# Kernel optimization log

Hardware: AMD Instinct MI355X
Metric: run time of the kernel (lower is better)

The kernel has to match this reference:

```python
import jax, jax.numpy as jnp
import numpy as np

N_ORDER = 64
SEQ_LEN = 4096
BATCH = 256


def _hippo_scale_buffers(N: int, L: int):
    """Build bilinear-discretized scaled-Legendre (HiPPO-LegS) transition buffers."""
    q = np.arange(N, dtype=np.float64)
    col, row = np.meshgrid(q, q)  # col[i,j]=j, row[i,j]=i
    r = 2 * q + 1
    M = -(np.where(row >= col, r, 0) - np.diag(q))
    T = np.sqrt(np.diag(2 * q + 1))
    A = T @ M @ np.linalg.inv(T)              # (N,N) continuous-time A
    Bv = np.sqrt(2 * q + 1)                   # diag(T) -> continuous-time B vector
    t = np.arange(1, L + 1, dtype=np.float64)
    A_sc = A[None, :, :] / t[:, None, None]   # (L,N,N)
    B_sc = Bv[None, :] / t[:, None]           # (L,N)
    I = np.eye(N, dtype=np.float64)
    Mm = I[None] - 0.5 * A_sc
    Nn = I[None] + 0.5 * A_sc
    A_d = np.linalg.solve(Mm, Nn)                        # (L,N,N)
    B_d = np.linalg.solve(Mm, B_sc[..., None])[..., 0]   # (L,N)
    return A_d.astype(np.float32), B_d.astype(np.float32)


def setup_inputs() -> dict:
    key = jax.random.key(0)
    inputs = jax.random.normal(key, (SEQ_LEN, BATCH), dtype=jnp.float32)
    A_np, B_np = _hippo_scale_buffers(N_ORDER, SEQ_LEN)
    return {
        "inputs": inputs,
        "A_stacked": jnp.asarray(A_np),   # (L,N,N)
        "B_stacked": jnp.asarray(B_np),   # (L,N)
    }


def reference(inputs, A_stacked, B_stacked):
    """x_t = A_t @ x_{t-1} + B_t * inputs_t, x_{-1} = 0. Returns (L, B, N)."""
    L = inputs.shape[0]
    # u[t, b, :] = inputs[t, b] * B_stacked[t, :]
    u = inputs[..., None] * B_stacked[:L, None, :]  # (L,B,N)

    def step(x, au):
        A_t, u_t = au                                  # (N,N), (B,N)
        x = u_t + jnp.einsum('ij,bj->bi', A_t, x)      # (B,N)
        return x, x

    x0 = jnp.zeros(u.shape[1:], dtype=u.dtype)
    _, xs = jax.lax.scan(step, x0, (A_stacked[:L], u))
    return xs  # (L,B,N)
```

## Files before the change

### kernel.cpp

```cpp
#include <hip/hip_runtime.h>
#include <cstdint>


#define TID ((int)threadIdx.x)

typedef _Float16 half8 __attribute__((ext_vector_type(8)));
typedef _Float16 half4v __attribute__((ext_vector_type(4)));
typedef float f32x4 __attribute__((ext_vector_type(4)));

constexpr int SUBL  = 16;
constexpr int PAD   = 68;

constexpr size_t WS_W = 0;
constexpr size_t WS_Q = 262144;
constexpr size_t WS_P = WS_Q + 1048576;
constexpr size_t WS_Z = WS_P + 262144;
constexpr size_t WS_H = WS_Z + 1048576;
constexpr size_t OLD_WS_FLOATS = WS_H + 1048576;

constexpr int SLOT   = 20480;
constexpr int APITCH = 144;
constexpr int AL_OFF = 9216;
constexpr int BV_OFF = 18432;
constexpr int U_OFF  = 18688;
constexpr size_t AWS_BYTES = (size_t)4096 * SLOT;

__device__ __forceinline__ void stage64x64(const float* __restrict__ g, float* __restrict__ l) {
#pragma unroll
  for (int r = 0; r < 4; ++r) {
    int id = TID + 256 * r;
    int i = id >> 4, j0 = (id & 15) << 2;
    *reinterpret_cast<float4*>(&l[i * PAD + j0]) =
        *reinterpret_cast<const float4*>(&g[i * 64 + j0]);
  }
}

__device__ __forceinline__ void matmul_tile(const float* __restrict__ Ml,
                                            const float* __restrict__ Al,
                                            float* __restrict__ Dl,
                                            int i_lo, int i_hi) {
  float acc[4][4];
#pragma unroll
  for (int a = 0; a < 4; ++a)
#pragma unroll
    for (int b = 0; b < 4; ++b) acc[a][b] = 0.f;
  const int j0 = i_hi << 2;
#pragma unroll
  for (int kq = 0; kq < 16; ++kq) {
    const int k0 = kq << 2;
    float4 mf[4], af[4];
#pragma unroll
    for (int a = 0; a < 4; ++a)
      mf[a] = *reinterpret_cast<const float4*>(&Ml[(i_lo + 16 * a) * PAD + k0]);
#pragma unroll
    for (int kk = 0; kk < 4; ++kk)
      af[kk] = *reinterpret_cast<const float4*>(&Al[(k0 + kk) * PAD + j0]);
#pragma unroll
    for (int a = 0; a < 4; ++a) {
      acc[a][0] += mf[a].x * af[0].x + mf[a].y * af[1].x + mf[a].z * af[2].x + mf[a].w * af[3].x;
      acc[a][1] += mf[a].x * af[0].y + mf[a].y * af[1].y + mf[a].z * af[2].y + mf[a].w * af[3].y;
      acc[a][2] += mf[a].x * af[0].z + mf[a].y * af[1].z + mf[a].z * af[2].z + mf[a].w * af[3].z;
      acc[a][3] += mf[a].x * af[0].w + mf[a].y * af[1].w + mf[a].z * af[2].w + mf[a].w * af[3].w;
    }
  }
#pragma unroll
  for (int a = 0; a < 4; ++a)
    *reinterpret_cast<float4*>(&Dl[(i_lo + 16 * a) * PAD + j0]) =
        make_float4(acc[a][0], acc[a][1], acc[a][2], acc[a][3]);
}

__global__ __launch_bounds__(256) void k1_fused(const float* __restrict__ Ag,
                                                const float* __restrict__ Bg,
                                                const float* __restrict__ inp,
                                                unsigned char* __restrict__ Aws,
                                                float* __restrict__ W,
                                                float* __restrict__ Qw) {
  __shared__ float Ms[2][64 * PAD];
  __shared__ float As[2][64 * PAD];
  __shared__ float Bvs[2][64];
  const int c = blockIdx.x;
  const int i_lo = TID & 15, i_hi = TID >> 4;
  const int r_i0 = TID >> 4;
  const int r_j0 = (TID & 15) << 2;

  for (int idx = TID; idx < 64 * PAD; idx += 256) Ms[0][idx] = 0.f;

  float4 pc[4];
  float4 bvc = make_float4(0.f, 0.f, 0.f, 0.f);
  {
    const float* g = Ag + (size_t)(c * SUBL + SUBL - 1) * 4096;
#pragma unroll
    for (int r = 0; r < 4; ++r)
      pc[r] = *reinterpret_cast<const float4*>(&g[(r_i0 + 16 * r) * 64 + r_j0]);
    if (TID < 16)
      bvc = *reinterpret_cast<const float4*>(&Bg[(size_t)(c * SUBL + SUBL - 1) * 64 + TID * 4]);
  }
  __syncthreads();
  if (TID < 64) Ms[0][TID * PAD + TID] = 1.f;
#pragma unroll
  for (int r = 0; r < 4; ++r)
    *reinterpret_cast<float4*>(&As[0][(r_i0 + 16 * r) * PAD + r_j0]) = pc[r];
  if (TID < 16) *reinterpret_cast<float4*>(&Bvs[0][TID * 4]) = bvc;
  __syncthreads();

  int cur = 0, ab = 0;
  for (int k = SUBL - 1; k >= 0; --k) {
    const int t = c * SUBL + k;
    unsigned char* slot = Aws + (size_t)t * SLOT;
    float4 pn[4];
    float4 bvn = make_float4(0.f, 0.f, 0.f, 0.f);
    if (k > 0) {
      const float* g = Ag + (size_t)(t - 1) * 4096;
#pragma unroll
      for (int r = 0; r < 4; ++r)
        pn[r] = *reinterpret_cast<const float4*>(&g[(r_i0 + 16 * r) * 64 + r_j0]);
      if (TID < 16)
        bvn = *reinterpret_cast<const float4*>(&Bg[(size_t)(t - 1) * 64 + TID * 4]);
    }
    if (TID >= 64 && TID < 128) {
      int q = TID - 64;
      *reinterpret_cast<float4*>(slot + U_OFF + q * 16) =
          *reinterpret_cast<const float4*>(inp + (size_t)t * 256 + q * 4);
    }
    if (TID < 16) *reinterpret_cast<float4*>(slot + BV_OFF + TID * 16) = bvc;
    if (TID < 64) {
      float wv = 0.f;
#pragma unroll
      for (int kq = 0; kq < 16; ++kq) {
        float4 m = *reinterpret_cast<const float4*>(&Ms[cur][TID * PAD + kq * 4]);
        float4 b = *reinterpret_cast<const float4*>(&Bvs[ab][kq * 4]);
        wv += m.x * b.x + m.y * b.y + m.z * b.z + m.w * b.w;
      }
      W[t * 64 + TID] = wv;
    }
#pragma unroll
    for (int r = 0; r < 4; ++r) {
      float vv[4] = {pc[r].x, pc[r].y, pc[r].z, pc[r].w};
      half4v hh, ll;
#pragma unroll
      for (int e = 0; e < 4; ++e) {
        _Float16 h = (_Float16)vv[e];
        hh[e] = h;
        ll[e] = (_Float16)(vv[e] - (float)h);
      }
      const int row = r_i0 + 16 * r;
      *reinterpret_cast<half4v*>(slot + row * APITCH + r_j0 * 2) = hh;
      *reinterpret_cast<half4v*>(slot + AL_OFF + row * APITCH + r_j0 * 2) = ll;
    }
    if (TID < 64) {
      half8 z = {};
      *reinterpret_cast<half8*>(slot + TID * APITCH + 128) = z;
      *reinterpret_cast<half8*>(slot + AL_OFF + TID * APITCH + 128) = z;
    }
    matmul_tile(Ms[cur], As[ab], Ms[cur ^ 1], i_lo, i_hi);
    if (k > 0) {
#pragma unroll
      for (int r = 0; r < 4; ++r)
        *reinterpret_cast<float4*>(&As[ab ^ 1][(r_i0 + 16 * r) * PAD + r_j0]) = pn[r];
      if (TID < 16) *reinterpret_cast<float4*>(&Bvs[ab ^ 1][TID * 4]) = bvn;
#pragma unroll
      for (int r = 0; r < 4; ++r) pc[r] = pn[r];
      bvc = bvn;
    }
    __syncthreads();
    cur ^= 1;
    ab ^= 1;
  }
#pragma unroll
  for (int r = 0; r < 4; ++r) {
    int id = TID + 256 * r;
    int i = id >> 4, j0 = (id & 15) << 2;
    *reinterpret_cast<float4*>(&Qw[(size_t)c * 4096 + i * 64 + j0]) =
        *reinterpret_cast<const float4*>(&Ms[cur][i * PAD + j0]);
  }
}

__global__ __launch_bounds__(256) void k1_suffix(const float* __restrict__ Ag,
                                                 const float* __restrict__ Bg,
                                                 float* __restrict__ W,
                                                 float* __restrict__ Qw) {
  __shared__ float Ms[2][64 * PAD];
  __shared__ float As[64 * PAD];
  __shared__ float Bvs[64];
  const int c = blockIdx.x;
  const int i_lo = TID & 15, i_hi = TID >> 4;
  for (int idx = TID; idx < 64 * PAD; idx += 256) Ms[0][idx] = 0.f;
  __syncthreads();
  if (TID < 64) Ms[0][TID * PAD + TID] = 1.f;
  int cur = 0;
  for (int k = SUBL - 1; k >= 0; --k) {
    const int t = c * SUBL + k;
    stage64x64(Ag + (size_t)t * 4096, As);
    if (TID < 16)
      *reinterpret_cast<float4*>(&Bvs[TID * 4]) =
          *reinterpret_cast<const float4*>(&Bg[t * 64 + TID * 4]);
    __syncthreads();
    if (TID < 64) {
      float wv = 0.f;
#pragma unroll
      for (int kq = 0; kq < 16; ++kq) {
        float4 m = *reinterpret_cast<const float4*>(&Ms[cur][TID * PAD + kq * 4]);
        float4 b = *reinterpret_cast<const float4*>(&Bvs[kq * 4]);
        wv += m.x * b.x + m.y * b.y + m.z * b.z + m.w * b.w;
      }
      W[t * 64 + TID] = wv;
    }
    matmul_tile(Ms[cur], As, Ms[cur ^ 1], i_lo, i_hi);
    __syncthreads();
    cur ^= 1;
  }
#pragma unroll
  for (int r = 0; r < 4; ++r) {
    int id = TID + 256 * r;
    int i = id >> 4, j0 = (id & 15) << 2;
    *reinterpret_cast<float4*>(&Qw[(size_t)c * 4096 + i * 64 + j0]) =
        *reinterpret_cast<const float4*>(&Ms[cur][i * PAD + j0]);
  }
}

__global__ __launch_bounds__(256) void k1b_combine(const float* __restrict__ Qw,
                                                   float* __restrict__ W,
                                                   float* __restrict__ Pw) {
  __shared__ float R[2][64 * PAD];
  __shared__ float Qs[64 * PAD];
  __shared__ float wm[16 * PAD];
  const int s = blockIdx.x;
  const int i_lo = TID & 15, i_hi = TID >> 4;
  int cur = 0;
  for (int m = 3; m >= 0; --m) {
    const int c = 4 * s + m;
    stage64x64(Qw + (size_t)c * 4096, Qs);
    {
      int tt = TID >> 4, i0 = (TID & 15) << 2;
      *reinterpret_cast<float4*>(&wm[tt * PAD + i0]) =
          *reinterpret_cast<const float4*>(&W[(size_t)(c * 16 + tt) * 64 + i0]);
    }
    __syncthreads();
    if (m < 3) {
      float acc[4] = {0.f, 0.f, 0.f, 0.f};
#pragma unroll
      for (int kq = 0; kq < 16; ++kq) {
        const int k0 = kq << 2;
        float4 wf = *reinterpret_cast<const float4*>(&wm[i_hi * PAD + k0]);
#pragma unroll
        for (int a = 0; a < 4; ++a) {
          float4 rf = *reinterpret_cast<const float4*>(&R[cur][(i_lo + 16 * a) * PAD + k0]);
          acc[a] += rf.x * wf.x + rf.y * wf.y + rf.z * wf.z + rf.w * wf.w;
        }
      }
#pragma unroll
      for (int a = 0; a < 4; ++a)
        W[(size_t)(c * 16 + i_hi) * 64 + i_lo + 16 * a] = acc[a];
      matmul_tile(R[cur], Qs, R[cur ^ 1], i_lo, i_hi);
    } else {
#pragma unroll
      for (int r = 0; r < 4; ++r) {
        int id = TID + 256 * r;
        int i = id >> 4, j0 = (id & 15) << 2;
        *reinterpret_cast<float4*>(&R[cur ^ 1][i * PAD + j0]) =
            *reinterpret_cast<const float4*>(&Qs[i * PAD + j0]);
      }
    }
    __syncthreads();
    cur ^= 1;
  }
#pragma unroll
  for (int r = 0; r < 4; ++r) {
    int id = TID + 256 * r;
    int i = id >> 4, j0 = (id & 15) << 2;
    *reinterpret_cast<float4*>(&Pw[(size_t)s * 4096 + i * 64 + j0]) =
        *reinterpret_cast<const float4*>(&R[cur][i * PAD + j0]);
  }
}

__global__ __launch_bounds__(256) void k1c_zgemm(const float* __restrict__ inp,
                                                 const float* __restrict__ W,
                                                 float* __restrict__ Zw) {
  __shared__ float inT[64 * PAD];
  __shared__ float wm[64 * PAD];
  const int s = blockIdx.x >> 2, g = blockIdx.x & 3;
  const int b0 = 64 * g, t0 = s * 64;
  const int i_lo = TID & 15, i_hi = TID >> 4;
#pragma unroll
  for (int r = 0; r < 4; ++r) {
    int id = TID + 256 * r;
    int tl = id >> 4, b4 = (id & 15) << 2;
    float4 v = *reinterpret_cast<const float4*>(&inp[(size_t)(t0 + tl) * 256 + b0 + b4]);
    inT[(b4 + 0) * PAD + tl] = v.x;
    inT[(b4 + 1) * PAD + tl] = v.y;
    inT[(b4 + 2) * PAD + tl] = v.z;
    inT[(b4 + 3) * PAD + tl] = v.w;
  }
#pragma unroll
  for (int r = 0; r < 4; ++r) {
    int id = TID + 256 * r;
    int tl = id >> 4, i0 = (id & 15) << 2;
    *reinterpret_cast<float4*>(&wm[tl * PAD + i0]) =
        *reinterpret_cast<const float4*>(&W[(size_t)(t0 + tl) * 64 + i0]);
  }
  __syncthreads();
  float acc[4][4];
#pragma unroll
  for (int a = 0; a < 4; ++a)
#pragma unroll
    for (int q = 0; q < 4; ++q) acc[a][q] = 0.f;
  const int j0c = i_hi << 2;
#pragma unroll
  for (int kq = 0; kq < 16; ++kq) {
    const int k0 = kq << 2;
    float4 bf[4], wf[4];
#pragma unroll
    for (int a = 0; a < 4; ++a)
      bf[a] = *reinterpret_cast<const float4*>(&inT[(i_lo + 16 * a) * PAD + k0]);
#pragma unroll
    for (int kk = 0; kk < 4; ++kk)
      wf[kk] = *reinterpret_cast<const float4*>(&wm[(k0 + kk) * PAD + j0c]);
#pragma unroll
    for (int a = 0; a < 4; ++a) {
      acc[a][0] += bf[a].x * wf[0].x + bf[a].y * wf[1].x + bf[a].z * wf[2].x + bf[a].w * wf[3].x;
      acc[a][1] += bf[a].x * wf[0].y + bf[a].y * wf[1].y + bf[a].z * wf[2].y + bf[a].w * wf[3].y;
      acc[a][2] += bf[a].x * wf[0].z + bf[a].y * wf[1].z + bf[a].z * wf[2].z + bf[a].w * wf[3].z;
      acc[a][3] += bf[a].x * wf[0].w + bf[a].y * wf[1].w + bf[a].z * wf[2].w + bf[a].w * wf[3].w;
    }
  }
  __syncthreads();
#pragma unroll
  for (int a = 0; a < 4; ++a)
    *reinterpret_cast<float4*>(&wm[(i_lo + 16 * a) * PAD + j0c]) =
        make_float4(acc[a][0], acc[a][1], acc[a][2], acc[a][3]);
  __syncthreads();
#pragma unroll
  for (int r = 0; r < 4; ++r) {
    int id = TID + 256 * r;
    int bl = id >> 4, i0 = (id & 15) << 2;
    *reinterpret_cast<float4*>(&Zw[(size_t)s * 16384 + (b0 + bl) * 64 + i0]) =
        *reinterpret_cast<const float4*>(&wm[bl * PAD + i0]);
  }
}

__global__ __launch_bounds__(256) void k2_carry(const float* __restrict__ Pw,
                                                const float* __restrict__ Zw,
                                                float* __restrict__ Hw) {
  __shared__ float Pt[64 * PAD];
  __shared__ float xb[4 * PAD];
  const int g = blockIdx.x;
  const int bl = TID >> 6, i = TID & 63;
  const int bg = 4 * g + bl;
  const int ir = TID >> 4, j0 = (TID & 15) << 2;
  for (int idx = TID; idx < 4 * PAD; idx += 256) xb[idx] = 0.f;
  float4 p0[4];
#pragma unroll
  for (int r = 0; r < 4; ++r)
    p0[r] = *reinterpret_cast<const float4*>(&Pw[(ir + 16 * r) * 64 + j0]);
  float zc = Zw[(size_t)bg * 64 + i];
#pragma unroll
  for (int r = 0; r < 4; ++r) {
    int row = ir + 16 * r;
    Pt[(j0 + 0) * PAD + row] = p0[r].x;
    Pt[(j0 + 1) * PAD + row] = p0[r].y;
    Pt[(j0 + 2) * PAD + row] = p0[r].z;
    Pt[(j0 + 3) * PAD + row] = p0[r].w;
  }
  __syncthreads();
  float h = 0.f;
  for (int s = 0; s < 64; ++s) {
    float4 pn[4];
    float zn = 0.f;
    if (s < 63) {
#pragma unroll
      for (int r = 0; r < 4; ++r)
        pn[r] = *reinterpret_cast<const float4*>(
            &Pw[(size_t)(s + 1) * 4096 + (ir + 16 * r) * 64 + j0]);
      zn = Zw[(size_t)(s + 1) * 16384 + bg * 64 + i];
    }
    Hw[(size_t)s * 16384 + bg * 64 + i] = h;
    float acc = zc;
#pragma unroll
    for (int jq = 0; jq < 16; ++jq) {
      const int jj = jq << 2;
      float4 xf = *reinterpret_cast<const float4*>(&xb[bl * PAD + jj]);
      acc += Pt[(jj + 0) * PAD + i] * xf.x + Pt[(jj + 1) * PAD + i] * xf.y +
             Pt[(jj + 2) * PAD + i] * xf.z + Pt[(jj + 3) * PAD + i] * xf.w;
    }
    h = acc;
    __syncthreads();
    xb[bl * PAD + i] = h;
    if (s < 63) {
#pragma unroll
      for (int r = 0; r < 4; ++r) {
        int row = ir + 16 * r;
        Pt[(j0 + 0) * PAD + row] = pn[r].x;
        Pt[(j0 + 1) * PAD + row] = pn[r].y;
        Pt[(j0 + 2) * PAD + row] = pn[r].z;
        Pt[(j0 + 3) * PAD + row] = pn[r].w;
      }
      zc = zn;
    }
    __syncthreads();
  }
}

__global__ __launch_bounds__(256) void k3_final(const float* __restrict__ Ag,
                                                const float* __restrict__ Bg,
                                                const float* __restrict__ inp,
                                                const float* __restrict__ Hw,
                                                float* __restrict__ out) {
  __shared__ float As[64 * PAD];
  __shared__ float xs[64 * PAD];
  __shared__ float Bvs[64];
  __shared__ float ins[64];
  const int s = blockIdx.x >> 2, g = blockIdx.x & 3;
  const int b0 = 64 * g;
  const int i_lo = TID & 15, i_hi = TID >> 4;
#pragma unroll
  for (int r = 0; r < 4; ++r) {
    int id = TID + 256 * r;
    int bl = id >> 4, i0 = (id & 15) << 2;
    *reinterpret_cast<float4*>(&xs[bl * PAD + i0]) =
        *reinterpret_cast<const float4*>(&Hw[(size_t)s * 16384 + (b0 + bl) * 64 + i0]);
  }
  for (int k = 0; k < 64; ++k) {
    const int t = s * 64 + k;
    stage64x64(Ag + (size_t)t * 4096, As);
    if (TID < 16)
      *reinterpret_cast<float4*>(&Bvs[TID * 4]) =
          *reinterpret_cast<const float4*>(&Bg[t * 64 + TID * 4]);
    if (TID >= 64 && TID < 80) {
      int q = TID - 64;
      *reinterpret_cast<float4*>(&ins[q * 4]) =
          *reinterpret_cast<const float4*>(&inp[(size_t)t * 256 + b0 + q * 4]);
    }
    __syncthreads();
    float acc[4][4];
#pragma unroll
    for (int a = 0; a < 4; ++a)
#pragma unroll
      for (int r = 0; r < 4; ++r) acc[a][r] = 0.f;
#pragma unroll
    for (int jq = 0; jq < 16; ++jq) {
      const int j0 = jq << 2;
      float4 af[4], xf[4];
#pragma unroll
      for (int a = 0; a < 4; ++a)
        af[a] = *reinterpret_cast<const float4*>(&As[(i_lo + 16 * a) * PAD + j0]);
#pragma unroll
      for (int r = 0; r < 4; ++r)
        xf[r] = *reinterpret_cast<const float4*>(&xs[(i_hi + 16 * r) * PAD + j0]);
#pragma unroll
      for (int a = 0; a < 4; ++a)
#pragma unroll
        for (int r = 0; r < 4; ++r)
          acc[a][r] += af[a].x * xf[r].x + af[a].y * xf[r].y + af[a].z * xf[r].z + af[a].w * xf[r].w;
    }
    float bv[4], ui[4];
#pragma unroll
    for (int a = 0; a < 4; ++a) bv[a] = Bvs[i_lo + 16 * a];
#pragma unroll
    for (int r = 0; r < 4; ++r) ui[r] = ins[i_hi + 16 * r];
#pragma unroll
    for (int a = 0; a < 4; ++a)
#pragma unroll
      for (int r = 0; r < 4; ++r) acc[a][r] += bv[a] * ui[r];
    __syncthreads();
#pragma unroll
    for (int r = 0; r < 4; ++r)
#pragma unroll
      for (int a = 0; a < 4; ++a)
        xs[(i_hi + 16 * r) * PAD + i_lo + 16 * a] = acc[a][r];
    __syncthreads();
#pragma unroll
    for (int r = 0; r < 4; ++r) {
      int id = TID + 256 * r;
      int bl = id >> 4, i0 = (id & 15) << 2;
      *reinterpret_cast<float4*>(&out[((size_t)t * 256 + b0 + bl) * 64 + i0]) =
          *reinterpret_cast<const float4*>(&xs[bl * PAD + i0]);
    }
  }
}

__device__ __forceinline__ void gload_lds16(const void* g, void* l) {
  __builtin_amdgcn_global_load_lds(
      (const __attribute__((address_space(1))) unsigned int*)g,
      (__attribute__((address_space(3))) unsigned int*)l, 16, 0, 0);
}

constexpr int XROWS  = 32;
constexpr int LDS_XH = 2 * SLOT;
constexpr int LDS_XL = LDS_XH + XROWS * APITCH;
constexpr int LDS_SZ = LDS_XL + XROWS * APITCH;

__global__ __launch_bounds__(256, 2) void k3_mfma(const unsigned char* __restrict__ Aws,
                                                  const float* __restrict__ Hw,
                                                  float* __restrict__ out) {
  __shared__ __align__(16) unsigned char sm[LDS_SZ];
  const int blk = blockIdx.x;
  const int s = (blk & 7) | ((blk >> 6) << 3);
  const int g = (blk >> 3) & 7;
  const int b0 = g << 5;
  const int lane = TID & 63, wave = TID >> 6;
  const int lm = lane & 15, quad = lane >> 4;
  const int wm = wave >> 1, wn = wave & 1;

#pragma unroll
  for (int r = 0; r < 2; ++r) {
    int id = TID + (r << 8);
    int bl = id >> 4, j0 = (id & 15) << 2;
    float4 v = *reinterpret_cast<const float4*>(
        &Hw[(size_t)s * 16384 + (size_t)(b0 + bl) * 64 + j0]);
    float vv[4] = {v.x, v.y, v.z, v.w};
    half4v hh, ll;
#pragma unroll
    for (int e = 0; e < 4; ++e) {
      _Float16 h = (_Float16)vv[e];
      hh[e] = h;
      ll[e] = (_Float16)(vv[e] - (float)h);
    }
    *reinterpret_cast<half4v*>(sm + LDS_XH + bl * APITCH + (j0 << 1)) = hh;
    *reinterpret_cast<half4v*>(sm + LDS_XL + bl * APITCH + (j0 << 1)) = ll;
  }

  const size_t t0 = (size_t)s * 64;
  {
    const unsigned char* gsl = Aws + t0 * SLOT;
#pragma unroll
    for (int r = 0; r < 5; ++r) {
      int off = ((r << 2) + wave) << 10;
      gload_lds16(gsl + off + lane * 16, sm + off);
    }
  }

  int aoff[2][2], xoffh[2], xoffl[2], woff[2];
#pragma unroll
  for (int mt = 0; mt < 2; ++mt)
#pragma unroll
    for (int kt = 0; kt < 2; ++kt)
      aoff[mt][kt] = ((wm << 5) + (mt << 4) + lm) * APITCH + (((kt << 5) + (quad << 3)) << 1);
#pragma unroll
  for (int kt = 0; kt < 2; ++kt) {
    int o = ((wn << 4) + lm) * APITCH + (((kt << 5) + (quad << 3)) << 1);
    xoffh[kt] = LDS_XH + o;
    xoffl[kt] = LDS_XL + o;
  }
#pragma unroll
  for (int mt = 0; mt < 2; ++mt)
    woff[mt] = ((wn << 4) + lm) * APITCH + (((wm << 5) + (mt << 4) + (quad << 2)) << 1);

  __syncthreads();

  int cur = 0;
  for (int k = 0; k < 64; ++k) {
    const unsigned char* ab = sm + cur * SLOT;
    if (k < 63) {
      const unsigned char* gsl = Aws + (t0 + k + 1) * SLOT;
      unsigned char* lb = sm + (cur ^ 1) * SLOT;
#pragma unroll
      for (int r = 0; r < 5; ++r) {
        int off = ((r << 2) + wave) << 10;
        gload_lds16(gsl + off + lane * 16, lb + off);
      }
    }
    half8 fa[2][2], fal[2][2], fxh[2], fxl[2];
#pragma unroll
    for (int mt = 0; mt < 2; ++mt)
#pragma unroll
      for (int kt = 0; kt < 2; ++kt) {
        fa[mt][kt]  = *reinterpret_cast<const half8*>(ab + aoff[mt][kt]);
        fal[mt][kt] = *reinterpret_cast<const half8*>(ab + AL_OFF + aoff[mt][kt]);
      }
#pragma unroll
    for (int kt = 0; kt < 2; ++kt) {
      fxh[kt] = *reinterpret_cast<const half8*>(sm + xoffh[kt]);
      fxl[kt] = *reinterpret_cast<const half8*>(sm + xoffl[kt]);
    }
    float4 bv[2];
#pragma unroll
    for (int mt = 0; mt < 2; ++mt)
      bv[mt] = *reinterpret_cast<const float4*>(
          ab + BV_OFF + (((wm << 5) + (mt << 4) + (quad << 2)) << 2));
    float uu = *reinterpret_cast<const float*>(
        ab + U_OFF + ((b0 + (wn << 4) + lm) << 2));

    f32x4 acc[2] = {};
#pragma unroll
    for (int mt = 0; mt < 2; ++mt)
#pragma unroll
      for (int kt = 0; kt < 2; ++kt) {
        acc[mt] = __builtin_amdgcn_mfma_f32_16x16x32_f16(fa[mt][kt],  fxh[kt], acc[mt], 0, 0, 0);
        acc[mt] = __builtin_amdgcn_mfma_f32_16x16x32_f16(fal[mt][kt], fxh[kt], acc[mt], 0, 0, 0);
        acc[mt] = __builtin_amdgcn_mfma_f32_16x16x32_f16(fa[mt][kt],  fxl[kt], acc[mt], 0, 0, 0);
      }
#pragma unroll
    for (int mt = 0; mt < 2; ++mt) {
      const float* bp = reinterpret_cast<const float*>(&bv[mt]);
#pragma unroll
      for (int e = 0; e < 4; ++e) acc[mt][e] += bp[e] * uu;
    }
    __syncthreads();
#pragma unroll
    for (int mt = 0; mt < 2; ++mt) {
      half4v hh, ll;
#pragma unroll
      for (int e = 0; e < 4; ++e) {
        float x = acc[mt][e];
        _Float16 h = (_Float16)x;
        hh[e] = h;
        ll[e] = (_Float16)(x - (float)h);
      }
      *reinterpret_cast<half4v*>(sm + LDS_XH + woff[mt]) = hh;
      *reinterpret_cast<half4v*>(sm + LDS_XL + woff[mt]) = ll;
      const int bglob = b0 + (wn << 4) + lm;
      const int irow = (wm << 5) + (mt << 4) + (quad << 2);
      *reinterpret_cast<float4*>(&out[(((t0 + k) << 8) + bglob) * 64 + irow]) =
          make_float4(acc[mt][0], acc[mt][1], acc[mt][2], acc[mt][3]);
    }
    __syncthreads();
    cur ^= 1;
  }
}

extern "C" void kernel_launch(void* const* d_in, const int* in_sizes, int n_in,
                              void* d_out, int out_size, void* d_ws, size_t ws_size,
                              hipStream_t stream) {
  const float* inputs = (const float*)d_in[0];
  const float* Ag     = (const float*)d_in[1];
  const float* Bg     = (const float*)d_in[2];
  float* out = (float*)d_out;

  const bool use_mfma = ws_size >= AWS_BYTES + OLD_WS_FLOATS * 4;
  unsigned char* Aws = (unsigned char*)d_ws;
  float* ws = (float*)((char*)d_ws + (use_mfma ? AWS_BYTES : 0));
  float* W  = ws + WS_W;
  float* Qw = ws + WS_Q;
  float* Pw = ws + WS_P;
  float* Zw = ws + WS_Z;
  float* Hw = ws + WS_H;

  if (use_mfma)
    k1_fused<<<256, 256, 0, stream>>>(Ag, Bg, inputs, Aws, W, Qw);
  else
    k1_suffix<<<256, 256, 0, stream>>>(Ag, Bg, W, Qw);
  k1b_combine<<<64, 256, 0, stream>>>(Qw, W, Pw);
  k1c_zgemm<<<256, 256, 0, stream>>>(inputs, W, Zw);
  k2_carry<<<64, 256, 0, stream>>>(Pw, Zw, Hw);
  if (use_mfma)
    k3_mfma<<<512, 256, 0, stream>>>(Aws, Hw, out);
  else
    k3_final<<<256, 256, 0, stream>>>(Ag, Bg, inputs, Hw, out);
}
```

Measured before the change: 581.7 us.

## Triple-buffer A slices and double-buffer state to halve barriers per step

Result: no change. 585.1 us (+0.6%).

```diff
diff --git a/kernel.cpp b/kernel.cpp
--- a/kernel.cpp
+++ b/kernel.cpp
@@ -341,13 +341,13 @@
 __global__ __launch_bounds__(256) void k2_carry(const float* __restrict__ Pw,
                                                 const float* __restrict__ Zw,
                                                 float* __restrict__ Hw) {
-  __shared__ float Pt[64 * PAD];
-  __shared__ float xb[4 * PAD];
+  __shared__ float Pt[2][64 * PAD];
+  __shared__ float xb[2][4 * PAD];
   const int g = blockIdx.x;
   const int bl = TID >> 6, i = TID & 63;
   const int bg = 4 * g + bl;
   const int ir = TID >> 4, j0 = (TID & 15) << 2;
-  for (int idx = TID; idx < 4 * PAD; idx += 256) xb[idx] = 0.f;
+  for (int idx = TID; idx < 4 * PAD; idx += 256) xb[0][idx] = 0.f;
   float4 p0[4];
 #pragma unroll
   for (int r = 0; r < 4; ++r)
@@ -356,14 +356,15 @@
 #pragma unroll
   for (int r = 0; r < 4; ++r) {
     int row = ir + 16 * r;
-    Pt[(j0 + 0) * PAD + row] = p0[r].x;
-    Pt[(j0 + 1) * PAD + row] = p0[r].y;
-    Pt[(j0 + 2) * PAD + row] = p0[r].z;
-    Pt[(j0 + 3) * PAD + row] = p0[r].w;
+    Pt[0][(j0 + 0) * PAD + row] = p0[r].x;
+    Pt[0][(j0 + 1) * PAD + row] = p0[r].y;
+    Pt[0][(j0 + 2) * PAD + row] = p0[r].z;
+    Pt[0][(j0 + 3) * PAD + row] = p0[r].w;
   }
   __syncthreads();
   float h = 0.f;
   for (int s = 0; s < 64; ++s) {
+    const int rb = s & 1, wb = rb ^ 1;
     float4 pn[4];
     float zn = 0.f;
     if (s < 63) {
@@ -378,21 +379,20 @@
 #pragma unroll
     for (int jq = 0; jq < 16; ++jq) {
       const int jj = jq << 2;
-      float4 xf = *reinterpret_cast<const float4*>(&xb[bl * PAD + jj]);
-      acc += Pt[(jj + 0) * PAD + i] * xf.x + Pt[(jj + 1) * PAD + i] * xf.y +
-             Pt[(jj + 2) * PAD + i] * xf.z + Pt[(jj + 3) * PAD + i] * xf.w;
+      float4 xf = *reinterpret_cast<const float4*>(&xb[rb][bl * PAD + jj]);
+      acc += Pt[rb][(jj + 0) * PAD + i] * xf.x + Pt[rb][(jj + 1) * PAD + i] * xf.y +
+             Pt[rb][(jj + 2) * PAD + i] * xf.z + Pt[rb][(jj + 3) * PAD + i] * xf.w;
     }
     h = acc;
-    __syncthreads();
-    xb[bl * PAD + i] = h;
+    xb[wb][bl * PAD + i] = h;
     if (s < 63) {
 #pragma unroll
       for (int r = 0; r < 4; ++r) {
         int row = ir + 16 * r;
-        Pt[(j0 + 0) * PAD + row] = pn[r].x;
-        Pt[(j0 + 1) * PAD + row] = pn[r].y;
-        Pt[(j0 + 2) * PAD + row] = pn[r].z;
-        Pt[(j0 + 3) * PAD + row] = pn[r].w;
+        Pt[wb][(j0 + 0) * PAD + row] = pn[r].x;
+        Pt[wb][(j0 + 1) * PAD + row] = pn[r].y;
+        Pt[wb][(j0 + 2) * PAD + row] = pn[r].z;
+        Pt[wb][(j0 + 3) * PAD + row] = pn[r].w;
       }
       zc = zn;
     }
@@ -485,9 +485,10 @@
 }
 
 constexpr int XROWS  = 32;
-constexpr int LDS_XH = 2 * SLOT;
-constexpr int LDS_XL = LDS_XH + XROWS * APITCH;
-constexpr int LDS_SZ = LDS_XL + XROWS * APITCH;
+constexpr int XHALF  = XROWS * APITCH;
+constexpr int XBUF   = 2 * XHALF;
+constexpr int LDS_X0 = 3 * SLOT;
+constexpr int LDS_SZ = LDS_X0 + 2 * XBUF;
 
 __global__ __launch_bounds__(256, 2) void k3_mfma(const unsigned char* __restrict__ Aws,
                                                   const float* __restrict__ Hw,
@@ -515,50 +516,54 @@
       hh[e] = h;
       ll[e] = (_Float16)(vv[e] - (float)h);
     }
-    *reinterpret_cast<half4v*>(sm + LDS_XH + bl * APITCH + (j0 << 1)) = hh;
-    *reinterpret_cast<half4v*>(sm + LDS_XL + bl * APITCH + (j0 << 1)) = ll;
+    *reinterpret_cast<half4v*>(sm + LDS_X0 + bl * APITCH + (j0 << 1)) = hh;
+    *reinterpret_cast<half4v*>(sm + LDS_X0 + XHALF + bl * APITCH + (j0 << 1)) = ll;
   }
 
   const size_t t0 = (size_t)s * 64;
-  {
-    const unsigned char* gsl = Aws + t0 * SLOT;
+#pragma unroll
+  for (int sl = 0; sl < 2; ++sl) {
+    const unsigned char* gsl = Aws + (t0 + sl) * SLOT;
 #pragma unroll
     for (int r = 0; r < 5; ++r) {
       int off = ((r << 2) + wave) << 10;
-      gload_lds16(gsl + off + lane * 16, sm + off);
-    }
-  }
-
-  int aoff[2][2], xoffh[2], xoffl[2], woff[2];
+      gload_lds16(gsl + off + lane * 16, sm + sl * SLOT + off);
+    }
+  }
+
+  int aoff[2][2], xoff[2], woff[2];
 #pragma unroll
   for (int mt = 0; mt < 2; ++mt)
 #pragma unroll
     for (int kt = 0; kt < 2; ++kt)
       aoff[mt][kt] = ((wm << 5) + (mt << 4) + lm) * APITCH + (((kt << 5) + (quad << 3)) << 1);
 #pragma unroll
-  for (int kt = 0; kt < 2; ++kt) {
-    int o = ((wn << 4) + lm) * APITCH + (((kt << 5) + (quad << 3)) << 1);
-    xoffh[kt] = LDS_XH + o;
-    xoffl[kt] = LDS_XL + o;
-  }
+  for (int kt = 0; kt < 2; ++kt)
+    xoff[kt] = ((wn << 4) + lm) * APITCH + (((kt << 5) + (quad << 3)) << 1);
 #pragma unroll
   for (int mt = 0; mt < 2; ++mt)
     woff[mt] = ((wn << 4) + lm) * APITCH + (((wm << 5) + (mt << 4) + (quad << 2)) << 1);
 
-  __syncthreads();
-
-  int cur = 0;
+  asm volatile("s_waitcnt vmcnt(5) lgkmcnt(0)" ::: "memory");
+  __builtin_amdgcn_s_barrier();
+  __builtin_amdgcn_sched_barrier(0);
+
+  int bufA = 0;
+  int xr = 0;
+#pragma unroll 1
   for (int k = 0; k < 64; ++k) {
-    const unsigned char* ab = sm + cur * SLOT;
-    if (k < 63) {
-      const unsigned char* gsl = Aws + (t0 + k + 1) * SLOT;
-      unsigned char* lb = sm + (cur ^ 1) * SLOT;
+    const unsigned char* ab = sm + bufA * SLOT;
+    if (k < 62) {
+      int nb = bufA + 2; if (nb >= 3) nb -= 3;
+      const unsigned char* gsl = Aws + (t0 + k + 2) * SLOT;
+      unsigned char* lb = sm + nb * SLOT;
 #pragma unroll
       for (int r = 0; r < 5; ++r) {
         int off = ((r << 2) + wave) << 10;
         gload_lds16(gsl + off + lane * 16, lb + off);
       }
     }
+    const unsigned char* xb = sm + LDS_X0 + xr * XBUF;
     half8 fa[2][2], fal[2][2], fxh[2], fxl[2];
 #pragma unroll
     for (int mt = 0; mt < 2; ++mt)
@@ -569,8 +574,8 @@
       }
 #pragma unroll
     for (int kt = 0; kt < 2; ++kt) {
-      fxh[kt] = *reinterpret_cast<const half8*>(sm + xoffh[kt]);
-      fxl[kt] = *reinterpret_cast<const half8*>(sm + xoffl[kt]);
+      fxh[kt] = *reinterpret_cast<const half8*>(xb + xoff[kt]);
+      fxl[kt] = *reinterpret_cast<const half8*>(xb + XHALF + xoff[kt]);
     }
     float4 bv[2];
 #pragma unroll
@@ -581,6 +586,7 @@
         ab + U_OFF + ((b0 + (wn << 4) + lm) << 2));
 
     f32x4 acc[2] = {};
+    __builtin_amdgcn_s_setprio(1);
 #pragma unroll
     for (int mt = 0; mt < 2; ++mt)
 #pragma unroll
@@ -589,13 +595,14 @@
         acc[mt] = __builtin_amdgcn_mfma_f32_16x16x32_f16(fal[mt][kt], fxh[kt], acc[mt], 0, 0, 0);
         acc[mt] = __builtin_amdgcn_mfma_f32_16x16x32_f16(fa[mt][kt],  fxl[kt], acc[mt], 0, 0, 0);
       }
+    __builtin_amdgcn_s_setprio(0);
 #pragma unroll
     for (int mt = 0; mt < 2; ++mt) {
       const float* bp = reinterpret_cast<const float*>(&bv[mt]);
 #pragma unroll
       for (int e = 0; e < 4; ++e) acc[mt][e] += bp[e] * uu;
     }
-    __syncthreads();
+    unsigned char* xw = sm + LDS_X0 + (xr ^ 1) * XBUF;
 #pragma unroll
     for (int mt = 0; mt < 2; ++mt) {
       half4v hh, ll;
@@ -606,15 +613,22 @@
         hh[e] = h;
         ll[e] = (_Float16)(x - (float)h);
       }
-      *reinterpret_cast<half4v*>(sm + LDS_XH + woff[mt]) = hh;
-      *reinterpret_cast<half4v*>(sm + LDS_XL + woff[mt]) = ll;
+      *reinterpret_cast<half4v*>(xw + woff[mt]) = hh;
+      *reinterpret_cast<half4v*>(xw + XHALF + woff[mt]) = ll;
       const int bglob = b0 + (wn << 4) + lm;
       const int irow = (wm << 5) + (mt << 4) + (quad << 2);
       *reinterpret_cast<float4*>(&out[(((t0 + k) << 8) + bglob) * 64 + irow]) =
           make_float4(acc[mt][0], acc[mt][1], acc[mt][2], acc[mt][3]);
     }
-    __syncthreads();
-    cur ^= 1;
+    if (k < 63) {
+      if (k == 0)      asm volatile("s_waitcnt vmcnt(7) lgkmcnt(0)" ::: "memory");
+      else if (k < 62) asm volatile("s_waitcnt vmcnt(9) lgkmcnt(0)" ::: "memory");
+      else             asm volatile("s_waitcnt vmcnt(4) lgkmcnt(0)" ::: "memory");
+      __builtin_amdgcn_s_barrier();
+      __builtin_amdgcn_sched_barrier(0);
+    }
+    bufA = (bufA + 1 == 3) ? 0 : bufA + 1;
+    xr ^= 1;
   }
 }
 
```
